# Optimization experiments

Measured on AMD Instinct MI355X. Metric: run time of the kernel, lower is better.

The kernel has to match this reference:

```python
import jax, jax.numpy as jnp
import numpy as np

N = 32768          # nodes
LEVELS = 4         # num_sign_hops + 1
NUM_FEATURES = 512
HIDDEN = 512
VQ_DIM = 64
CODEBOOK_SIZE = 4096
VQ_WEIGHT = 0.25   # commitment_weight


def setup_inputs() -> dict:
    key = jax.random.key(0)
    ks = jax.random.split(key, 11)
    s = 0.02
    return {
        "x": jax.random.normal(ks[0], (N, LEVELS, NUM_FEATURES), jnp.float32),
        # per-level encoder: Linear(F,512) -> ReLU -> Linear(512,D)
        "enc_w1": jax.random.normal(ks[1], (LEVELS, NUM_FEATURES, HIDDEN), jnp.float32) * s,
        "enc_b1": jnp.zeros((LEVELS, HIDDEN), jnp.float32),
        "enc_w2": jax.random.normal(ks[2], (LEVELS, HIDDEN, VQ_DIM), jnp.float32) * s,
        "enc_b2": jnp.zeros((LEVELS, VQ_DIM), jnp.float32),
        # per-level decoder: Linear(D,512) -> ReLU -> Linear(512,F)
        "dec_w1": jax.random.normal(ks[3], (LEVELS, VQ_DIM, HIDDEN), jnp.float32) * s,
        "dec_b1": jnp.zeros((LEVELS, HIDDEN), jnp.float32),
        "dec_w2": jax.random.normal(ks[4], (LEVELS, HIDDEN, NUM_FEATURES), jnp.float32) * s,
        "dec_b2": jnp.zeros((LEVELS, NUM_FEATURES), jnp.float32),
        # per-level EMA codebooks (constants w.r.t. gradient in the torch module)
        "codebook": jax.random.normal(ks[5], (LEVELS, CODEBOOK_SIZE, VQ_DIM), jnp.float32),
    }


def reference(x, enc_w1, enc_b1, enc_w2, enc_b2,
              dec_w1, dec_b1, dec_w2, dec_b2, codebook):
    # Faithful to Quantizer.forward (eval mode: dropout = identity; EMA codebook
    # update is a training-time side effect, not part of the returned math).
    L = x.shape[1]
    total_mse = jnp.float32(0.0)
    commit_last = jnp.float32(0.0)
    for l in range(L):  # small fixed level count, structurally distinct params
        xl = x[:, l, :]                                   # [N, F]
        h = jax.nn.relu(xl @ enc_w1[l] + enc_b1[l])       # [N, 512]
        z = h @ enc_w2[l] + enc_b2[l]                     # [N, D]
        cb = codebook[l]                                  # [K, D]
        # squared euclidean distances [N, K] (cdist^2 via expansion)
        d = ((z * z).sum(-1, keepdims=True)
             - 2.0 * (z @ cb.T)
             + (cb * cb).sum(-1)[None, :])
        idx = jnp.argmin(d, axis=-1)                      # [N]
        q = cb[idx]                                       # [N, D] codebook lookup
        # commitment loss: mse(stop_grad(quantize), z) * weight
        commit = VQ_WEIGHT * jnp.mean((jax.lax.stop_gradient(q) - z) ** 2)
        # straight-through estimator
        quant = z + jax.lax.stop_gradient(q - z)
        h2 = jax.nn.relu(quant @ dec_w1[l] + dec_b1[l])   # [N, 512]
        x_hat = h2 @ dec_w2[l] + dec_b2[l]                # [N, F]
        total_mse = total_mse + jnp.mean((x_hat - xl) ** 2)
        commit_last = commit  # original returns LAST level's commit_loss / levels
    return (total_mse / L, commit_last / L)
```

## Files before the change

### kernel.cpp

```cpp
#include <hip/hip_runtime.h>

#define NS 32768
#define NLEV 4
#define NF 512
#define HID 512
#define VQD 64
#define CBS 4096

typedef __attribute__((ext_vector_type(8))) short bf16x8;
typedef __attribute__((ext_vector_type(4))) float f32x4;

__device__ inline unsigned short f2bf(float f) {
    unsigned int u = __float_as_uint(f);
    unsigned int r = (u + 0x7FFFu + ((u >> 16) & 1u)) >> 16;
    return (unsigned short)r;
}
__device__ inline float bf2f(unsigned short s) {
    return __uint_as_float(((unsigned int)s) << 16);
}

__device__ __forceinline__ void gl16(const void* g, void* l) {
    __builtin_amdgcn_global_load_lds(
        (const __attribute__((address_space(1))) unsigned int*)g,
        (__attribute__((address_space(3))) unsigned int*)l, 16, 0, 0);
}


__global__ void transpose_all(const float* __restrict__ ew1, const float* __restrict__ ew2,
                              const float* __restrict__ dw1, const float* __restrict__ dw2,
                              unsigned short* __restrict__ ew1t, unsigned short* __restrict__ ew2t,
                              unsigned short* __restrict__ dw1t, unsigned short* __restrict__ dw2t) {
    long i = (long)blockIdx.x * 256 + threadIdx.x;
    const long s1 = (long)NLEV * NF * HID;
    const long s2 = (long)NLEV * HID * VQD;
    const long s3 = (long)NLEV * VQD * HID;
    const long s4 = (long)NLEV * HID * NF;
    const float* src;
    unsigned short* dst;
    int R, C;
    if (i < s1) { src = ew1; dst = ew1t; R = NF; C = HID; }
    else if (i < s1 + s2) { i -= s1; src = ew2; dst = ew2t; R = HID; C = VQD; }
    else if (i < s1 + s2 + s3) { i -= s1 + s2; src = dw1; dst = dw1t; R = VQD; C = HID; }
    else if (i < s1 + s2 + s3 + s4) { i -= s1 + s2 + s3; src = dw2; dst = dw2t; R = HID; C = NF; }
    else return;
    int r = (int)(i % R);
    long t = i / R;
    int c = (int)(t % C);
    int b = (int)(t / C);
    dst[i] = f2bf(src[((long)b * R + r) * C + c]);
}

__global__ void cb_prep(const float* __restrict__ cb, unsigned short* __restrict__ cbb,
                        float* __restrict__ cbn) {
    int i = blockIdx.x * 256 + threadIdx.x;
    if (i >= NLEV * CBS) return;
    const float* row = cb + (long)i * VQD;
    float s = 0.f;
    for (int k = 0; k < VQD; k++) {
        float v = row[k];
        s += v * v;
        cbb[(long)i * VQD + k] = f2bf(v);
    }
    cbn[i] = s;
}

__global__ void xconv(const float* __restrict__ x, unsigned short* __restrict__ xb) {
    long i = (long)blockIdx.x * 256 + threadIdx.x;
    int l = (int)(i / ((long)NS * (NF / 8)));
    long rem = i % ((long)NS * (NF / 8));
    int n = (int)(rem >> 6);
    int f8 = ((int)rem & 63) * 8;
    const float* src = x + ((long)n * NLEV + l) * NF + f8;
    float4 f0 = *(const float4*)src;
    float4 f1 = *(const float4*)(src + 4);
    short t[8];
    t[0] = (short)f2bf(f0.x); t[1] = (short)f2bf(f0.y); t[2] = (short)f2bf(f0.z); t[3] = (short)f2bf(f0.w);
    t[4] = (short)f2bf(f1.x); t[5] = (short)f2bf(f1.y); t[6] = (short)f2bf(f1.z); t[7] = (short)f2bf(f1.w);
    *(int4*)(xb + ((long)l * NS + n) * NF + f8) = *(const int4*)t;
}

template <int NT, int NTOT, int RELU, int OUT_MODE, int GATHER>
__global__ __launch_bounds__(256) void gemm128(
    const unsigned short* __restrict__ Ab, long astride, long abatch,
    const int* __restrict__ idx,
    const unsigned short* __restrict__ Bt, long bbatch,
    const float* __restrict__ bias, long biasbatch,
    unsigned short* __restrict__ Cb, long cbatch,
    const unsigned short* __restrict__ Xref, long xbatch,
    float* __restrict__ accum, int K) {
    constexpr int BN = NT * 32;
    constexpr int NPAN = NTOT / BN;
    constexpr int BNP = BN + 8;
    __shared__ __align__(16) short smem[2 * 128 * 32 + 2 * BN * 32];
    short* As = smem;
    short* Bs = smem + 2 * 128 * 32;
    __shared__ float red[4];

    const int bid = blockIdx.x;
    const int inner = bid % (256 * NPAN);
    const int lvl = bid / (256 * NPAN);
    constexpr int CHUNK = 8 * NPAN;
    const int mblk = (inner / CHUNK) * 8 + (inner % CHUNK) / NPAN;
    const int n_blk = inner % NPAN;

    Ab += (long)lvl * abatch;
    Bt += (long)lvl * bbatch;
    bias += (long)lvl * biasbatch;
    if (OUT_MODE == 0) Cb += (long)lvl * cbatch;
    if (OUT_MODE == 2) Xref += (long)lvl * xbatch;
    if (GATHER) idx += (long)lvl * NS;

    const int tid = threadIdx.x;
    const int m0 = mblk * 128;
    const int n0 = n_blk * BN;
    const int wave = tid >> 6, lane = tid & 63, quad = lane >> 4, lr = lane & 15;
    const int wm = wave >> 1, wn = wave & 1;
    const int lrow = lane >> 2;
    const int lcol = (lane & 3) * 8;

    long idx0 = 0, idx1 = 0;
    if (GATHER) {
        idx0 = idx[m0 + wave * 16 + lrow];
        idx1 = idx[m0 + 64 + wave * 16 + lrow];
    }

    f32x4 acc[4][NT];
#pragma unroll
    for (int i = 0; i < 4; i++)
#pragma unroll
        for (int j = 0; j < NT; j++) acc[i][j] = (f32x4){0.f, 0.f, 0.f, 0.f};

    for (int k0 = 0; k0 < K; k0 += 64) {
#pragma unroll
        for (int p = 0; p < 2; p++) {
            const int kk = k0 + p * 32;
            if (GATHER) {
                gl16(Ab + idx0 * K + kk + lcol, &As[p * 4096 + (wave * 16) * 32]);
                gl16(Ab + idx1 * K + kk + lcol, &As[p * 4096 + (64 + wave * 16) * 32]);
            } else {
                const unsigned short* ga = Ab + (long)(m0 + wave * 16 + lrow) * astride + kk + lcol;
                gl16(ga, &As[p * 4096 + (wave * 16) * 32]);
                gl16(ga + 64 * astride, &As[p * 4096 + (64 + wave * 16) * 32]);
            }
            const unsigned short* gb = Bt + (long)(n0 + wave * 16 + lrow) * K + kk + lcol;
            gl16(gb, &Bs[p * BN * 32 + (wave * 16) * 32]);
            if (NT == 4) gl16(gb + 64 * (long)K, &Bs[p * BN * 32 + (64 + wave * 16) * 32]);
        }
        __syncthreads();
#pragma unroll
        for (int p = 0; p < 2; p++) {
            bf16x8 af[4], bfr[NT];
#pragma unroll
            for (int mt = 0; mt < 4; mt++)
                af[mt] = *(const bf16x8*)&As[p * 4096 + (wm * 64 + mt * 16 + lr) * 32 + quad * 8];
#pragma unroll
            for (int nt = 0; nt < NT; nt++)
                bfr[nt] = *(const bf16x8*)&Bs[p * BN * 32 + (wn * NT * 16 + nt * 16 + lr) * 32 + quad * 8];
#pragma unroll
            for (int mt = 0; mt < 4; mt++)
#pragma unroll
                for (int nt = 0; nt < NT; nt++)
                    acc[mt][nt] = __builtin_amdgcn_mfma_f32_16x16x32_bf16(af[mt], bfr[nt], acc[mt][nt], 0, 0, 0);
        }
        __syncthreads();
    }

    float bvs[NT];
#pragma unroll
    for (int nt = 0; nt < NT; nt++) bvs[nt] = bias[n0 + wn * NT * 16 + nt * 16 + lr];

    if (OUT_MODE == 2) {
        float lsum = 0.f;
#pragma unroll
        for (int nt = 0; nt < NT; nt++) {
            int col = n0 + wn * NT * 16 + nt * 16 + lr;
#pragma unroll
            for (int mt = 0; mt < 4; mt++) {
#pragma unroll
                for (int r = 0; r < 4; r++) {
                    int row = m0 + wm * 64 + mt * 16 + quad * 4 + r;
                    float v = acc[mt][nt][r] + bvs[nt];
                    float d = v - bf2f(Xref[(long)row * NTOT + col]);
                    lsum += d * d;
                }
            }
        }
#pragma unroll
        for (int off = 32; off; off >>= 1) lsum += __shfl_down(lsum, off, 64);
        if (lane == 0) red[wave] = lsum;
        __syncthreads();
        if (tid == 0) atomicAdd(accum, red[0] + red[1] + red[2] + red[3]);
    } else {
        short* Ct = smem;
#pragma unroll
        for (int p = 0; p < 2; p++) {
            __syncthreads();
            if (wm == p) {
#pragma unroll
                for (int nt = 0; nt < NT; nt++) {
                    int cl = wn * NT * 16 + nt * 16 + lr;
#pragma unroll
                    for (int mt = 0; mt < 4; mt++) {
#pragma unroll
                        for (int r = 0; r < 4; r++) {
                            int rl = mt * 16 + quad * 4 + r;
                            float v = acc[mt][nt][r] + bvs[nt];
                            if (RELU) v = v > 0.f ? v : 0.f;
                            Ct[rl * BNP + cl] = (short)f2bf(v);
                        }
                    }
                }
            }
            __syncthreads();
            constexpr int PER = (64 * BN / 8) / 256;
#pragma unroll
            for (int j = 0; j < PER; j++) {
                int id = j * 256 + tid;
                int row = id / (BN / 8);
                int seg = id % (BN / 8);
                short tmp[8];
                *(int4*)tmp = *(const int4*)&Ct[row * BNP + seg * 8];
                *(int4*)&Cb[(long)(m0 + p * 64 + row) * NTOT + n0 + seg * 8] = *(const int4*)tmp;
            }
        }
    }
}

__global__ __launch_bounds__(256) void enc2_vq(
    const unsigned short* __restrict__ hb, const unsigned short* __restrict__ ew2t,
    const float* __restrict__ eb2, const unsigned short* __restrict__ cbb,
    const float* __restrict__ cbn, int* __restrict__ idxo, float* __restrict__ accum) {
    __shared__ __align__(16) short As[2 * 128 * 32];
    __shared__ __align__(16) short Bs[2 * 64 * 32];
    __shared__ float znp[2][128];
    __shared__ float zn2[128];
    __shared__ float cred;

    const int lvl = blockIdx.y;
    hb += (long)lvl * NS * HID;
    ew2t += (long)lvl * VQD * HID;
    eb2 += (long)lvl * VQD;
    cbb += (long)lvl * CBS * VQD;
    cbn += (long)lvl * CBS;
    idxo += (long)lvl * NS;

    const int tid = threadIdx.x;
    const int m0 = blockIdx.x * 128;
    const int wave = tid >> 6, lane = tid & 63, quad = lane >> 4, lr = lane & 15;
    const int wm = wave >> 1, wn = wave & 1;
    const int lrow = lane >> 2, lcol = (lane & 3) * 8;

    if (tid == 0) cred = 0.f;

    f32x4 acc[4][2];
#pragma unroll
    for (int i = 0; i < 4; i++)
#pragma unroll
        for (int j = 0; j < 2; j++) acc[i][j] = (f32x4){0.f, 0.f, 0.f, 0.f};

    for (int k0 = 0; k0 < HID; k0 += 64) {
#pragma unroll
        for (int p = 0; p < 2; p++) {
            const int kk = k0 + p * 32;
            const unsigned short* ga = hb + (long)(m0 + wave * 16 + lrow) * HID + kk + lcol;
            gl16(ga, &As[p * 4096 + (wave * 16) * 32]);
            gl16(ga + 64 * HID, &As[p * 4096 + (64 + wave * 16) * 32]);
            const unsigned short* gb = ew2t + (long)(wave * 16 + lrow) * HID + kk + lcol;
            gl16(gb, &Bs[p * 2048 + (wave * 16) * 32]);
        }
        __syncthreads();
#pragma unroll
        for (int p = 0; p < 2; p++) {
            bf16x8 af[4], bfr[2];
#pragma unroll
            for (int mt = 0; mt < 4; mt++)
                af[mt] = *(const bf16x8*)&As[p * 4096 + (wm * 64 + mt * 16 + lr) * 32 + quad * 8];
#pragma unroll
            for (int nt = 0; nt < 2; nt++)
                bfr[nt] = *(const bf16x8*)&Bs[p * 2048 + (wn * 32 + nt * 16 + lr) * 32 + quad * 8];
#pragma unroll
            for (int mt = 0; mt < 4; mt++)
#pragma unroll
                for (int nt = 0; nt < 2; nt++)
                    acc[mt][nt] = __builtin_amdgcn_mfma_f32_16x16x32_bf16(af[mt], bfr[nt], acc[mt][nt], 0, 0, 0);
        }
        __syncthreads();
    }

    short* Zs = As;
    float bvs[2] = {eb2[wn * 32 + lr], eb2[wn * 32 + 16 + lr]};
#pragma unroll
    for (int mt = 0; mt < 4; mt++)
#pragma unroll
        for (int r = 0; r < 4; r++) {
            int row = wm * 64 + mt * 16 + quad * 4 + r;
#pragma unroll
            for (int nt = 0; nt < 2; nt++) {
                float v = acc[mt][nt][r] + bvs[nt];
                Zs[wn * 4096 + row * 32 + nt * 16 + lr] = (short)f2bf(v);
            }
        }
    __syncthreads();

    {
        int row = tid >> 1, p = tid & 1;
        const short* zr = &Zs[p * 4096 + row * 32];
        float s = 0.f;
#pragma unroll
        for (int j = 0; j < 32; j++) {
            float f = bf2f((unsigned short)zr[j]);
            s += f * f;
        }
        znp[p][row] = s;
    }
    bf16x8 a[2][2];
#pragma unroll
    for (int h = 0; h < 2; h++)
#pragma unroll
        for (int p = 0; p < 2; p++)
            a[h][p] = *(const bf16x8*)&Zs[p * 4096 + (h * 64 + wave * 16 + lr) * 32 + quad * 8];
    __syncthreads();
    if (tid < 128) zn2[tid] = znp[0][tid] + znp[1][tid];

    short* Cs = Bs;
    float minv[2][4] = {{1e30f, 1e30f, 1e30f, 1e30f}, {1e30f, 1e30f, 1e30f, 1e30f}};
    int mini[2][4] = {{0, 0, 0, 0}, {0, 0, 0, 0}};

    for (int nb = 0; nb < CBS; nb += 64) {
        __syncthreads();
#pragma unroll
        for (int i = 0; i < 2; i++) {
            int s = i * 4 + wave;
            int p = s >> 2;
            int r0 = (s & 3) * 16;
            gl16(cbb + (long)(nb + r0 + lrow) * VQD + p * 32 + lcol, &Cs[s * 512]);
        }
        __syncthreads();
#pragma unroll
        for (int nt = 0; nt < 4; nt++) {
            bf16x8 b0 = *(const bf16x8*)&Cs[(nt * 16 + lr) * 32 + quad * 8];
            bf16x8 b1 = *(const bf16x8*)&Cs[2048 + (nt * 16 + lr) * 32 + quad * 8];
            int n = nb + nt * 16 + lr;
            float cn = cbn[n];
#pragma unroll
            for (int h = 0; h < 2; h++) {
                f32x4 d4 = {0.f, 0.f, 0.f, 0.f};
                d4 = __builtin_amdgcn_mfma_f32_16x16x32_bf16(a[h][0], b0, d4, 0, 0, 0);
                d4 = __builtin_amdgcn_mfma_f32_16x16x32_bf16(a[h][1], b1, d4, 0, 0, 0);
#pragma unroll
                for (int r = 0; r < 4; r++) {
                    float d = cn - 2.0f * d4[r];
                    if (d < minv[h][r]) {
                        minv[h][r] = d;
                        mini[h][r] = n;
                    }
                }
            }
        }
    }

    float csum = 0.f;
#pragma unroll
    for (int h = 0; h < 2; h++)
#pragma unroll
        for (int r = 0; r < 4; r++) {
            float v = minv[h][r];
            int ix = mini[h][r];
#pragma unroll
            for (int off = 8; off; off >>= 1) {
                float ov = __shfl_xor(v, off, 64);
                int oi = __shfl_xor(ix, off, 64);
                if (ov < v || (ov == v && oi < ix)) {
                    v = ov;
                    ix = oi;
                }
            }
            if (lr == 0) {
                int row = h * 64 + wave * 16 + quad * 4 + r;
                idxo[m0 + row] = ix;
                csum += v + zn2[row];
            }
        }
    if (lvl == NLEV - 1) {
        if (lr == 0) atomicAdd(&cred, csum);
        __syncthreads();
        if (tid == 0) atomicAdd(accum + 1, cred);
    }
}

__global__ void finalize_k(const float* __restrict__ accum, float* __restrict__ out) {
    out[0] = accum[0] / ((float)NS * NF * NLEV);
    out[1] = 0.25f * accum[1] / ((float)NS * VQD * NLEV);
}

extern "C" void kernel_launch(void* const* d_in, const int* in_sizes, int n_in, void* d_out,
                              int out_size, void* d_ws, size_t ws_size, hipStream_t stream) {
    const float* x = (const float*)d_in[0];
    const float* enc_w1 = (const float*)d_in[1];
    const float* enc_b1 = (const float*)d_in[2];
    const float* enc_w2 = (const float*)d_in[3];
    const float* enc_b2 = (const float*)d_in[4];
    const float* dec_w1 = (const float*)d_in[5];
    const float* dec_b1 = (const float*)d_in[6];
    const float* dec_w2 = (const float*)d_in[7];
    const float* dec_b2 = (const float*)d_in[8];
    const float* cb = (const float*)d_in[9];

    char* ws = (char*)d_ws;
    size_t o = 0;
    float* accum = (float*)(ws + o); o += 256;
    unsigned short* enc_w1t = (unsigned short*)(ws + o); o += (size_t)NLEV * HID * NF * 2;
    unsigned short* enc_w2t = (unsigned short*)(ws + o); o += (size_t)NLEV * VQD * HID * 2;
    unsigned short* dec_w1t = (unsigned short*)(ws + o); o += (size_t)NLEV * HID * VQD * 2;
    unsigned short* dec_w2t = (unsigned short*)(ws + o); o += (size_t)NLEV * NF * HID * 2;
    unsigned short* cbb = (unsigned short*)(ws + o); o += (size_t)NLEV * CBS * VQD * 2;
    float* cbn = (float*)(ws + o); o += (size_t)NLEV * CBS * 4;
    unsigned short* xb = (unsigned short*)(ws + o); o += (size_t)NLEV * NS * NF * 2;
    unsigned short* hb = (unsigned short*)(ws + o); o += (size_t)NLEV * NS * HID * 2;
    int* idxp = (int*)(ws + o); o += (size_t)NLEV * NS * 4;

    hipMemsetAsync(accum, 0, 8, stream);

    transpose_all<<<(2 * NLEV * NF * HID + 2 * NLEV * HID * VQD + 255) / 256, 256, 0, stream>>>(
        enc_w1, enc_w2, dec_w1, dec_w2, enc_w1t, enc_w2t, dec_w1t, dec_w2t);
    cb_prep<<<(NLEV * CBS + 255) / 256, 256, 0, stream>>>(cb, cbb, cbn);
    xconv<<<(int)(((long)NLEV * NS * (NF / 8) + 255) / 256), 256, 0, stream>>>(x, xb);

    const int gBig = 256 * (HID / 128) * NLEV;

    gemm128<4, HID, 1, 0, 0><<<gBig, 256, 0, stream>>>(
        xb, NF, (long)NS * NF, nullptr,
        enc_w1t, (long)HID * NF, enc_b1, HID,
        hb, (long)NS * HID, nullptr, 0, nullptr, NF);
    enc2_vq<<<dim3(NS / 128, NLEV), 256, 0, stream>>>(hb, enc_w2t, enc_b2, cbb, cbn, idxp, accum);
    gemm128<4, HID, 1, 0, 1><<<gBig, 256, 0, stream>>>(
        cbb, 0, (long)CBS * VQD, idxp,
        dec_w1t, (long)HID * VQD, dec_b1, HID,
        hb, (long)NS * HID, nullptr, 0, nullptr, VQD);
    gemm128<4, NF, 0, 2, 0><<<gBig, 256, 0, stream>>>(
        hb, HID, (long)NS * HID, nullptr,
        dec_w2t, (long)NF * HID, dec_b2, NF,
        nullptr, 0, xb, (long)NS * NF, accum, HID);

    finalize_k<<<1, 1, 0, stream>>>(accum, (float*)d_out);
}
```

Measured before the change: 835.6 us.

## Fuse encoder MLP+VQ and decoder MLP+loss into two LDS-resident kernels

Replaces the four-kernel GEMM chain with two fused kernels. Each 128-row tile keeps its hidden activations (128x512 bf16) in LDS, so the [N,512] hidden buffer is never written to or read back from global memory. The kernels use 512 threads per block and double-buffered global-to-LDS staging, prefetching the next stage while the current one computes. The cost is 128KB+ of LDS per block, which limits occupancy to one block per CU, and far fewer blocks (1024 per launch) with less latency hiding.

```diff
diff --git a/kernel.cpp b/kernel.cpp
--- a/kernel.cpp
+++ b/kernel.cpp
@@ -9,6 +9,8 @@
 
 typedef __attribute__((ext_vector_type(8))) short bf16x8;
 typedef __attribute__((ext_vector_type(4))) float f32x4;
+
+#define MFMA16(a, b, c) __builtin_amdgcn_mfma_f32_16x16x32_bf16(a, b, c, 0, 0, 0)
 
 __device__ inline unsigned short f2bf(float f) {
     unsigned int u = __float_as_uint(f);
@@ -79,312 +81,323 @@
     *(int4*)(xb + ((long)l * NS + n) * NF + f8) = *(const int4*)t;
 }
 
-template <int NT, int NTOT, int RELU, int OUT_MODE, int GATHER>
-__global__ __launch_bounds__(256) void gemm128(
-    const unsigned short* __restrict__ Ab, long astride, long abatch,
-    const int* __restrict__ idx,
-    const unsigned short* __restrict__ Bt, long bbatch,
-    const float* __restrict__ bias, long biasbatch,
-    unsigned short* __restrict__ Cb, long cbatch,
-    const unsigned short* __restrict__ Xref, long xbatch,
-    float* __restrict__ accum, int K) {
-    constexpr int BN = NT * 32;
-    constexpr int NPAN = NTOT / BN;
-    constexpr int BNP = BN + 8;
-    __shared__ __align__(16) short smem[2 * 128 * 32 + 2 * BN * 32];
-    short* As = smem;
-    short* Bs = smem + 2 * 128 * 32;
-    __shared__ float red[4];
-
-    const int bid = blockIdx.x;
-    const int inner = bid % (256 * NPAN);
-    const int lvl = bid / (256 * NPAN);
-    constexpr int CHUNK = 8 * NPAN;
-    const int mblk = (inner / CHUNK) * 8 + (inner % CHUNK) / NPAN;
-    const int n_blk = inner % NPAN;
-
-    Ab += (long)lvl * abatch;
-    Bt += (long)lvl * bbatch;
-    bias += (long)lvl * biasbatch;
-    if (OUT_MODE == 0) Cb += (long)lvl * cbatch;
-    if (OUT_MODE == 2) Xref += (long)lvl * xbatch;
-    if (GATHER) idx += (long)lvl * NS;
-
-    const int tid = threadIdx.x;
-    const int m0 = mblk * 128;
-    const int n0 = n_blk * BN;
-    const int wave = tid >> 6, lane = tid & 63, quad = lane >> 4, lr = lane & 15;
-    const int wm = wave >> 1, wn = wave & 1;
-    const int lrow = lane >> 2;
-    const int lcol = (lane & 3) * 8;
-
-    long idx0 = 0, idx1 = 0;
-    if (GATHER) {
-        idx0 = idx[m0 + wave * 16 + lrow];
-        idx1 = idx[m0 + 64 + wave * 16 + lrow];
-    }
-
-    f32x4 acc[4][NT];
-#pragma unroll
-    for (int i = 0; i < 4; i++)
-#pragma unroll
-        for (int j = 0; j < NT; j++) acc[i][j] = (f32x4){0.f, 0.f, 0.f, 0.f};
-
-    for (int k0 = 0; k0 < K; k0 += 64) {
-#pragma unroll
-        for (int p = 0; p < 2; p++) {
-            const int kk = k0 + p * 32;
-            if (GATHER) {
-                gl16(Ab + idx0 * K + kk + lcol, &As[p * 4096 + (wave * 16) * 32]);
-                gl16(Ab + idx1 * K + kk + lcol, &As[p * 4096 + (64 + wave * 16) * 32]);
-            } else {
-                const unsigned short* ga = Ab + (long)(m0 + wave * 16 + lrow) * astride + kk + lcol;
-                gl16(ga, &As[p * 4096 + (wave * 16) * 32]);
-                gl16(ga + 64 * astride, &As[p * 4096 + (64 + wave * 16) * 32]);
-            }
-            const unsigned short* gb = Bt + (long)(n0 + wave * 16 + lrow) * K + kk + lcol;
-            gl16(gb, &Bs[p * BN * 32 + (wave * 16) * 32]);
-            if (NT == 4) gl16(gb + 64 * (long)K, &Bs[p * BN * 32 + (64 + wave * 16) * 32]);
-        }
-        __syncthreads();
-#pragma unroll
-        for (int p = 0; p < 2; p++) {
-            bf16x8 af[4], bfr[NT];
-#pragma unroll
-            for (int mt = 0; mt < 4; mt++)
-                af[mt] = *(const bf16x8*)&As[p * 4096 + (wm * 64 + mt * 16 + lr) * 32 + quad * 8];
-#pragma unroll
-            for (int nt = 0; nt < NT; nt++)
-                bfr[nt] = *(const bf16x8*)&Bs[p * BN * 32 + (wn * NT * 16 + nt * 16 + lr) * 32 + quad * 8];
-#pragma unroll
-            for (int mt = 0; mt < 4; mt++)
-#pragma unroll
-                for (int nt = 0; nt < NT; nt++)
-                    acc[mt][nt] = __builtin_amdgcn_mfma_f32_16x16x32_bf16(af[mt], bfr[nt], acc[mt][nt], 0, 0, 0);
-        }
-        __syncthreads();
-    }
-
-    float bvs[NT];
-#pragma unroll
-    for (int nt = 0; nt < NT; nt++) bvs[nt] = bias[n0 + wn * NT * 16 + nt * 16 + lr];
-
-    if (OUT_MODE == 2) {
-        float lsum = 0.f;
-#pragma unroll
-        for (int nt = 0; nt < NT; nt++) {
-            int col = n0 + wn * NT * 16 + nt * 16 + lr;
-#pragma unroll
-            for (int mt = 0; mt < 4; mt++) {
-#pragma unroll
-                for (int r = 0; r < 4; r++) {
-                    int row = m0 + wm * 64 + mt * 16 + quad * 4 + r;
-                    float v = acc[mt][nt][r] + bvs[nt];
-                    float d = v - bf2f(Xref[(long)row * NTOT + col]);
-                    lsum += d * d;
-                }
-            }
-        }
-#pragma unroll
-        for (int off = 32; off; off >>= 1) lsum += __shfl_down(lsum, off, 64);
-        if (lane == 0) red[wave] = lsum;
-        __syncthreads();
-        if (tid == 0) atomicAdd(accum, red[0] + red[1] + red[2] + red[3]);
-    } else {
-        short* Ct = smem;
-#pragma unroll
-        for (int p = 0; p < 2; p++) {
-            __syncthreads();
-            if (wm == p) {
-#pragma unroll
-                for (int nt = 0; nt < NT; nt++) {
-                    int cl = wn * NT * 16 + nt * 16 + lr;
-#pragma unroll
-                    for (int mt = 0; mt < 4; mt++) {
-#pragma unroll
-                        for (int r = 0; r < 4; r++) {
-                            int rl = mt * 16 + quad * 4 + r;
-                            float v = acc[mt][nt][r] + bvs[nt];
-                            if (RELU) v = v > 0.f ? v : 0.f;
-                            Ct[rl * BNP + cl] = (short)f2bf(v);
-                        }
-                    }
-                }
-            }
-            __syncthreads();
-            constexpr int PER = (64 * BN / 8) / 256;
-#pragma unroll
-            for (int j = 0; j < PER; j++) {
-                int id = j * 256 + tid;
-                int row = id / (BN / 8);
-                int seg = id % (BN / 8);
-                short tmp[8];
-                *(int4*)tmp = *(const int4*)&Ct[row * BNP + seg * 8];
-                *(int4*)&Cb[(long)(m0 + p * 64 + row) * NTOT + n0 + seg * 8] = *(const int4*)tmp;
-            }
-        }
-    }
-}
-
-__global__ __launch_bounds__(256) void enc2_vq(
-    const unsigned short* __restrict__ hb, const unsigned short* __restrict__ ew2t,
-    const float* __restrict__ eb2, const unsigned short* __restrict__ cbb,
+__global__ __launch_bounds__(512) void enc_fused(
+    const unsigned short* __restrict__ xb, const unsigned short* __restrict__ w1t,
+    const float* __restrict__ b1, const unsigned short* __restrict__ w2t,
+    const float* __restrict__ b2, const unsigned short* __restrict__ cbb,
     const float* __restrict__ cbn, int* __restrict__ idxo, float* __restrict__ accum) {
-    __shared__ __align__(16) short As[2 * 128 * 32];
-    __shared__ __align__(16) short Bs[2 * 64 * 32];
+    __shared__ __align__(16) short Hs[16 * 4096];
+    __shared__ __align__(16) short Zst[2 * 2048];
     __shared__ float znp[2][128];
     __shared__ float zn2[128];
     __shared__ float cred;
 
     const int lvl = blockIdx.y;
-    hb += (long)lvl * NS * HID;
-    ew2t += (long)lvl * VQD * HID;
-    eb2 += (long)lvl * VQD;
+    const int m0 = blockIdx.x * 128;
+    xb += (long)lvl * NS * NF;
+    w1t += (long)lvl * HID * NF;
+    b1 += (long)lvl * HID;
+    w2t += (long)lvl * VQD * HID;
+    b2 += (long)lvl * VQD;
     cbb += (long)lvl * CBS * VQD;
     cbn += (long)lvl * CBS;
     idxo += (long)lvl * NS;
 
     const int tid = threadIdx.x;
-    const int m0 = blockIdx.x * 128;
     const int wave = tid >> 6, lane = tid & 63, quad = lane >> 4, lr = lane & 15;
-    const int wm = wave >> 1, wn = wave & 1;
-    const int lrow = lane >> 2, lcol = (lane & 3) * 8;
+    const int wm = wave >> 2, wn = wave & 3;
+    const int lrow = lane >> 2;
+    const int lcol = (lane & 3) * 8;
 
     if (tid == 0) cred = 0.f;
 
-    f32x4 acc[4][2];
-#pragma unroll
-    for (int i = 0; i < 4; i++)
-#pragma unroll
-        for (int j = 0; j < 2; j++) acc[i][j] = (f32x4){0.f, 0.f, 0.f, 0.f};
-
-    for (int k0 = 0; k0 < HID; k0 += 64) {
-#pragma unroll
-        for (int p = 0; p < 2; p++) {
-            const int kk = k0 + p * 32;
-            const unsigned short* ga = hb + (long)(m0 + wave * 16 + lrow) * HID + kk + lcol;
-            gl16(ga, &As[p * 4096 + (wave * 16) * 32]);
-            gl16(ga + 64 * HID, &As[p * 4096 + (64 + wave * 16) * 32]);
-            const unsigned short* gb = ew2t + (long)(wave * 16 + lrow) * HID + kk + lcol;
-            gl16(gb, &Bs[p * 2048 + (wave * 16) * 32]);
-        }
-        __syncthreads();
-#pragma unroll
-        for (int p = 0; p < 2; p++) {
-            bf16x8 af[4], bfr[2];
-#pragma unroll
-            for (int mt = 0; mt < 4; mt++)
-                af[mt] = *(const bf16x8*)&As[p * 4096 + (wm * 64 + mt * 16 + lr) * 32 + quad * 8];
-#pragma unroll
-            for (int nt = 0; nt < 2; nt++)
-                bfr[nt] = *(const bf16x8*)&Bs[p * 2048 + (wn * 32 + nt * 16 + lr) * 32 + quad * 8];
-#pragma unroll
-            for (int mt = 0; mt < 4; mt++)
-#pragma unroll
-                for (int nt = 0; nt < 2; nt++)
-                    acc[mt][nt] = __builtin_amdgcn_mfma_f32_16x16x32_bf16(af[mt], bfr[nt], acc[mt][nt], 0, 0, 0);
-        }
-        __syncthreads();
-    }
-
-    short* Zs = As;
-    float bvs[2] = {eb2[wn * 32 + lr], eb2[wn * 32 + 16 + lr]};
-#pragma unroll
-    for (int mt = 0; mt < 4; mt++)
-#pragma unroll
-        for (int r = 0; r < 4; r++) {
-            int row = wm * 64 + mt * 16 + quad * 4 + r;
-#pragma unroll
-            for (int nt = 0; nt < 2; nt++) {
-                float v = acc[mt][nt][r] + bvs[nt];
-                Zs[wn * 4096 + row * 32 + nt * 16 + lr] = (short)f2bf(v);
-            }
-        }
+    f32x4 acc[4][4][2];
+#pragma unroll
+    for (int j = 0; j < 4; j++)
+#pragma unroll
+        for (int mt = 0; mt < 4; mt++) {
+            acc[j][mt][0] = (f32x4){0.f, 0.f, 0.f, 0.f};
+            acc[j][mt][1] = (f32x4){0.f, 0.f, 0.f, 0.f};
+        }
+
+    const unsigned short* ga = xb + (long)(m0 + wave * 16 + lrow) * NF + lcol;
+    auto stage1 = [&](int s) {
+        const int pi = s & 1;
+        gl16(ga + s * 32, &Hs[pi * 4096 + wave * 16 * 32]);
+#pragma unroll
+        for (int j = 0; j < 4; j++)
+            gl16(w1t + (long)(j * 128 + wave * 16 + lrow) * NF + s * 32 + lcol,
+                 &Hs[(2 + 2 * j + pi) * 4096 + wave * 16 * 32]);
+    };
+    stage1(0);
+#pragma unroll 2
+    for (int s = 0; s < 16; s++) {
+        __syncthreads();
+        if (s < 15) stage1(s + 1);
+        const int pi = s & 1;
+        bf16x8 af[4];
+#pragma unroll
+        for (int mt = 0; mt < 4; mt++)
+            af[mt] = *(const bf16x8*)&Hs[pi * 4096 + (wm * 64 + mt * 16 + lr) * 32 + quad * 8];
+#pragma unroll
+        for (int j = 0; j < 4; j++) {
+            bf16x8 bf0 = *(const bf16x8*)&Hs[(2 + 2 * j + pi) * 4096 + (wn * 32 + lr) * 32 + quad * 8];
+            bf16x8 bf1 = *(const bf16x8*)&Hs[(2 + 2 * j + pi) * 4096 + (wn * 32 + 16 + lr) * 32 + quad * 8];
+#pragma unroll
+            for (int mt = 0; mt < 4; mt++) {
+                acc[j][mt][0] = MFMA16(af[mt], bf0, acc[j][mt][0]);
+                acc[j][mt][1] = MFMA16(af[mt], bf1, acc[j][mt][1]);
+            }
+        }
+    }
     __syncthreads();
-
+#pragma unroll
+    for (int j = 0; j < 4; j++) {
+        float bv0 = b1[j * 128 + wn * 32 + lr];
+        float bv1 = b1[j * 128 + wn * 32 + 16 + lr];
+        short* hs = &Hs[(4 * j + wn) * 4096];
+#pragma unroll
+        for (int mt = 0; mt < 4; mt++)
+#pragma unroll
+            for (int r = 0; r < 4; r++) {
+                int row = wm * 64 + mt * 16 + quad * 4 + r;
+                float v0 = acc[j][mt][0][r] + bv0; v0 = v0 > 0.f ? v0 : 0.f;
+                float v1 = acc[j][mt][1][r] + bv1; v1 = v1 > 0.f ? v1 : 0.f;
+                hs[row * 32 + lr] = (short)f2bf(v0);
+                hs[row * 32 + 16 + lr] = (short)f2bf(v1);
+            }
+    }
+
+    f32x4 az[4];
+#pragma unroll
+    for (int mt = 0; mt < 4; mt++) az[mt] = (f32x4){0.f, 0.f, 0.f, 0.f};
+    auto stageZ = [&](int s) {
+        if (wave < 4)
+            gl16(w2t + (long)(wave * 16 + lrow) * HID + s * 32 + lcol,
+                 &Zst[(s & 1) * 2048 + wave * 16 * 32]);
+    };
+    stageZ(0);
+#pragma unroll 2
+    for (int s = 0; s < 16; s++) {
+        __syncthreads();
+        if (s < 15) stageZ(s + 1);
+        bf16x8 bz = *(const bf16x8*)&Zst[(s & 1) * 2048 + (wn * 16 + lr) * 32 + quad * 8];
+#pragma unroll
+        for (int mt = 0; mt < 4; mt++) {
+            bf16x8 af = *(const bf16x8*)&Hs[s * 4096 + (wm * 64 + mt * 16 + lr) * 32 + quad * 8];
+            az[mt] = MFMA16(af, bz, az[mt]);
+        }
+    }
+    __syncthreads();
     {
+        float bz0 = b2[wn * 16 + lr];
+        const int col = wn * 16 + lr;
+        short* zs = &Hs[(col >> 5) * 4096];
+        const int c32 = col & 31;
+#pragma unroll
+        for (int mt = 0; mt < 4; mt++)
+#pragma unroll
+            for (int r = 0; r < 4; r++) {
+                int row = wm * 64 + mt * 16 + quad * 4 + r;
+                zs[row * 32 + c32] = (short)f2bf(az[mt][r] + bz0);
+            }
+    }
+    __syncthreads();
+
+    auto stageC = [&](int t) {
+        gl16(cbb + (long)(t * 64 + wn * 16 + lrow) * VQD + wm * 32 + lcol,
+             &Hs[(2 + (t & 1)) * 4096 + wm * 2048 + wn * 512]);
+    };
+    stageC(0);
+    if (tid < 256) {
         int row = tid >> 1, p = tid & 1;
-        const short* zr = &Zs[p * 4096 + row * 32];
-        float s = 0.f;
-#pragma unroll
-        for (int j = 0; j < 32; j++) {
-            float f = bf2f((unsigned short)zr[j]);
-            s += f * f;
-        }
-        znp[p][row] = s;
-    }
-    bf16x8 a[2][2];
-#pragma unroll
-    for (int h = 0; h < 2; h++)
-#pragma unroll
-        for (int p = 0; p < 2; p++)
-            a[h][p] = *(const bf16x8*)&Zs[p * 4096 + (h * 64 + wave * 16 + lr) * 32 + quad * 8];
+        const short* zr = &Hs[p * 4096 + row * 32];
+        float s2 = 0.f;
+#pragma unroll
+        for (int j2 = 0; j2 < 32; j2++) {
+            float f = bf2f((unsigned short)zr[j2]);
+            s2 += f * f;
+        }
+        znp[p][row] = s2;
+    }
+    bf16x8 a0 = *(const bf16x8*)&Hs[(wave * 16 + lr) * 32 + quad * 8];
+    bf16x8 a1 = *(const bf16x8*)&Hs[4096 + (wave * 16 + lr) * 32 + quad * 8];
     __syncthreads();
     if (tid < 128) zn2[tid] = znp[0][tid] + znp[1][tid];
 
-    short* Cs = Bs;
-    float minv[2][4] = {{1e30f, 1e30f, 1e30f, 1e30f}, {1e30f, 1e30f, 1e30f, 1e30f}};
-    int mini[2][4] = {{0, 0, 0, 0}, {0, 0, 0, 0}};
-
-    for (int nb = 0; nb < CBS; nb += 64) {
-        __syncthreads();
-#pragma unroll
-        for (int i = 0; i < 2; i++) {
-            int s = i * 4 + wave;
-            int p = s >> 2;
-            int r0 = (s & 3) * 16;
-            gl16(cbb + (long)(nb + r0 + lrow) * VQD + p * 32 + lcol, &Cs[s * 512]);
-        }
-        __syncthreads();
+    float minv[4] = {1e30f, 1e30f, 1e30f, 1e30f};
+    int mini[4] = {0, 0, 0, 0};
+#pragma unroll 2
+    for (int t = 0; t < CBS / 64; t++) {
+        if (t) __syncthreads();
+        if (t < CBS / 64 - 1) stageC(t + 1);
+        const short* Cb = &Hs[(2 + (t & 1)) * 4096];
 #pragma unroll
         for (int nt = 0; nt < 4; nt++) {
-            bf16x8 b0 = *(const bf16x8*)&Cs[(nt * 16 + lr) * 32 + quad * 8];
-            bf16x8 b1 = *(const bf16x8*)&Cs[2048 + (nt * 16 + lr) * 32 + quad * 8];
-            int n = nb + nt * 16 + lr;
+            bf16x8 c0 = *(const bf16x8*)&Cb[(nt * 16 + lr) * 32 + quad * 8];
+            bf16x8 c1 = *(const bf16x8*)&Cb[2048 + (nt * 16 + lr) * 32 + quad * 8];
+            f32x4 d4 = {0.f, 0.f, 0.f, 0.f};
+            d4 = MFMA16(a0, c0, d4);
+            d4 = MFMA16(a1, c1, d4);
+            int n = t * 64 + nt * 16 + lr;
             float cn = cbn[n];
 #pragma unroll
-            for (int h = 0; h < 2; h++) {
-                f32x4 d4 = {0.f, 0.f, 0.f, 0.f};
-                d4 = __builtin_amdgcn_mfma_f32_16x16x32_bf16(a[h][0], b0, d4, 0, 0, 0);
-                d4 = __builtin_amdgcn_mfma_f32_16x16x32_bf16(a[h][1], b1, d4, 0, 0, 0);
-#pragma unroll
-                for (int r = 0; r < 4; r++) {
-                    float d = cn - 2.0f * d4[r];
-                    if (d < minv[h][r]) {
-                        minv[h][r] = d;
-                        mini[h][r] = n;
-                    }
-                }
+            for (int r = 0; r < 4; r++) {
+                float d = fmaf(-2.f, d4[r], cn);
+                if (d < minv[r]) { minv[r] = d; mini[r] = n; }
             }
         }
     }
 
     float csum = 0.f;
 #pragma unroll
-    for (int h = 0; h < 2; h++)
-#pragma unroll
-        for (int r = 0; r < 4; r++) {
-            float v = minv[h][r];
-            int ix = mini[h][r];
-#pragma unroll
-            for (int off = 8; off; off >>= 1) {
-                float ov = __shfl_xor(v, off, 64);
-                int oi = __shfl_xor(ix, off, 64);
-                if (ov < v || (ov == v && oi < ix)) {
-                    v = ov;
-                    ix = oi;
-                }
-            }
-            if (lr == 0) {
-                int row = h * 64 + wave * 16 + quad * 4 + r;
-                idxo[m0 + row] = ix;
-                csum += v + zn2[row];
-            }
-        }
+    for (int r = 0; r < 4; r++) {
+        float v = minv[r];
+        int ix = mini[r];
+#pragma unroll
+        for (int off = 8; off; off >>= 1) {
+            float ov = __shfl_xor(v, off, 64);
+            int oi = __shfl_xor(ix, off, 64);
+            if (ov < v || (ov == v && oi < ix)) { v = ov; ix = oi; }
+        }
+        if (lr == 0) {
+            int row = wave * 16 + quad * 4 + r;
+            idxo[m0 + row] = ix;
+            csum += v + zn2[row];
+        }
+    }
     if (lvl == NLEV - 1) {
         if (lr == 0) atomicAdd(&cred, csum);
         __syncthreads();
         if (tid == 0) atomicAdd(accum + 1, cred);
+    }
+}
+
+__global__ __launch_bounds__(512) void dec_fused(
+    const unsigned short* __restrict__ cbb, const int* __restrict__ idx,
+    const unsigned short* __restrict__ w1t, const float* __restrict__ b1,
+    const unsigned short* __restrict__ w2t, const float* __restrict__ b2,
+    const unsigned short* __restrict__ xref, float* __restrict__ accum) {
+    __shared__ __align__(16) short Hs[16 * 4096];
+    __shared__ __align__(16) short Bst[2 * 4096];
+    __shared__ float red[8];
+
+    const int lvl = blockIdx.y;
+    const int m0 = blockIdx.x * 128;
+    cbb += (long)lvl * CBS * VQD;
+    idx += (long)lvl * NS;
+    w1t += (long)lvl * HID * VQD;
+    b1 += (long)lvl * HID;
+    w2t += (long)lvl * NF * HID;
+    b2 += (long)lvl * NF;
+    xref += (long)lvl * NS * NF;
+
+    const int tid = threadIdx.x;
+    const int wave = tid >> 6, lane = tid & 63, quad = lane >> 4, lr = lane & 15;
+    const int wm = wave >> 2, wn = wave & 3;
+    const int lrow = lane >> 2;
+    const int lcol = (lane & 3) * 8;
+
+    const long idxv = idx[m0 + wave * 16 + lrow];
+
+    auto stageD = [&](int j) {
+#pragma unroll
+        for (int p = 0; p < 2; p++) {
+            gl16(cbb + idxv * VQD + p * 32 + lcol, &Hs[(4 * j + p) * 4096 + wave * 16 * 32]);
+            gl16(w1t + (long)(j * 128 + wave * 16 + lrow) * VQD + p * 32 + lcol,
+                 &Hs[(4 * j + 2 + p) * 4096 + wave * 16 * 32]);
+        }
+    };
+    stageD(0);
+#pragma unroll
+    for (int j = 0; j < 4; j++) {
+        f32x4 acc[4][2];
+#pragma unroll
+        for (int mt = 0; mt < 4; mt++) {
+            acc[mt][0] = (f32x4){0.f, 0.f, 0.f, 0.f};
+            acc[mt][1] = (f32x4){0.f, 0.f, 0.f, 0.f};
+        }
+        __syncthreads();
+        if (j < 3) stageD(j + 1);
+#pragma unroll
+        for (int p = 0; p < 2; p++) {
+            bf16x8 bf0 = *(const bf16x8*)&Hs[(4 * j + 2 + p) * 4096 + (wn * 32 + lr) * 32 + quad * 8];
+            bf16x8 bf1 = *(const bf16x8*)&Hs[(4 * j + 2 + p) * 4096 + (wn * 32 + 16 + lr) * 32 + quad * 8];
+#pragma unroll
+            for (int mt = 0; mt < 4; mt++) {
+                bf16x8 af = *(const bf16x8*)&Hs[(4 * j + p) * 4096 + (wm * 64 + mt * 16 + lr) * 32 + quad * 8];
+                acc[mt][0] = MFMA16(af, bf0, acc[mt][0]);
+                acc[mt][1] = MFMA16(af, bf1, acc[mt][1]);
+            }
+        }
+        __syncthreads();
+        float bv0 = b1[j * 128 + wn * 32 + lr];
+        float bv1 = b1[j * 128 + wn * 32 + 16 + lr];
+        short* hs = &Hs[(4 * j + wn) * 4096];
+#pragma unroll
+        for (int mt = 0; mt < 4; mt++)
+#pragma unroll
+            for (int r = 0; r < 4; r++) {
+                int row = wm * 64 + mt * 16 + quad * 4 + r;
+                float v0 = acc[mt][0][r] + bv0; v0 = v0 > 0.f ? v0 : 0.f;
+                float v1 = acc[mt][1][r] + bv1; v1 = v1 > 0.f ? v1 : 0.f;
+                hs[row * 32 + lr] = (short)f2bf(v0);
+                hs[row * 32 + 16 + lr] = (short)f2bf(v1);
+            }
+    }
+
+    auto stageB = [&](int g) {
+        gl16(w2t + (long)((g >> 4) * 128 + wave * 16 + lrow) * HID + (g & 15) * 32 + lcol,
+             &Bst[(g & 1) * 4096 + wave * 16 * 32]);
+    };
+    stageB(0);
+    float lsum = 0.f;
+    f32x4 acc2[4][2];
+#pragma unroll
+    for (int mt = 0; mt < 4; mt++) {
+        acc2[mt][0] = (f32x4){0.f, 0.f, 0.f, 0.f};
+        acc2[mt][1] = (f32x4){0.f, 0.f, 0.f, 0.f};
+    }
+#pragma unroll 2
+    for (int g = 0; g < 64; g++) {
+        __syncthreads();
+        if (g < 63) stageB(g + 1);
+        const int s = g & 15;
+        bf16x8 bf0 = *(const bf16x8*)&Bst[(g & 1) * 4096 + (wn * 32 + lr) * 32 + quad * 8];
+        bf16x8 bf1 = *(const bf16x8*)&Bst[(g & 1) * 4096 + (wn * 32 + 16 + lr) * 32 + quad * 8];
+#pragma unroll
+        for (int mt = 0; mt < 4; mt++) {
+            bf16x8 af = *(const bf16x8*)&Hs[s * 4096 + (wm * 64 + mt * 16 + lr) * 32 + quad * 8];
+            acc2[mt][0] = MFMA16(af, bf0, acc2[mt][0]);
+            acc2[mt][1] = MFMA16(af, bf1, acc2[mt][1]);
+        }
+        if (s == 15) {
+            const int jj = g >> 4;
+            float bv0 = b2[jj * 128 + wn * 32 + lr];
+            float bv1 = b2[jj * 128 + wn * 32 + 16 + lr];
+#pragma unroll
+            for (int mt = 0; mt < 4; mt++)
+#pragma unroll
+                for (int r = 0; r < 4; r++) {
+                    long row = m0 + wm * 64 + mt * 16 + quad * 4 + r;
+                    int c0 = jj * 128 + wn * 32 + lr;
+                    float v0 = acc2[mt][0][r] + bv0 - bf2f(xref[row * NF + c0]);
+                    float v1 = acc2[mt][1][r] + bv1 - bf2f(xref[row * NF + c0 + 16]);
+                    lsum += v0 * v0 + v1 * v1;
+                    acc2[mt][0][r] = 0.f;
+                    acc2[mt][1][r] = 0.f;
+                }
+        }
+    }
+#pragma unroll
+    for (int off = 32; off; off >>= 1) lsum += __shfl_down(lsum, off, 64);
+    if (lane == 0) red[wave] = lsum;
+    __syncthreads();
+    if (tid == 0) {
+        float s2 = 0.f;
+#pragma unroll
+        for (int w = 0; w < 8; w++) s2 += red[w];
+        atomicAdd(accum, s2);
     }
 }
 
@@ -416,7 +429,6 @@
     unsigned short* cbb = (unsigned short*)(ws + o); o += (size_t)NLEV * CBS * VQD * 2;
     float* cbn = (float*)(ws + o); o += (size_t)NLEV * CBS * 4;
     unsigned short* xb = (unsigned short*)(ws + o); o += (size_t)NLEV * NS * NF * 2;
-    unsigned short* hb = (unsigned short*)(ws + o); o += (size_t)NLEV * NS * HID * 2;
     int* idxp = (int*)(ws + o); o += (size_t)NLEV * NS * 4;
 
     hipMemsetAsync(accum, 0, 8, stream);
@@ -426,21 +438,10 @@
     cb_prep<<<(NLEV * CBS + 255) / 256, 256, 0, stream>>>(cb, cbb, cbn);
     xconv<<<(int)(((long)NLEV * NS * (NF / 8) + 255) / 256), 256, 0, stream>>>(x, xb);
 
-    const int gBig = 256 * (HID / 128) * NLEV;
-
-    gemm128<4, HID, 1, 0, 0><<<gBig, 256, 0, stream>>>(
-        xb, NF, (long)NS * NF, nullptr,
-        enc_w1t, (long)HID * NF, enc_b1, HID,
-        hb, (long)NS * HID, nullptr, 0, nullptr, NF);
-    enc2_vq<<<dim3(NS / 128, NLEV), 256, 0, stream>>>(hb, enc_w2t, enc_b2, cbb, cbn, idxp, accum);
-    gemm128<4, HID, 1, 0, 1><<<gBig, 256, 0, stream>>>(
-        cbb, 0, (long)CBS * VQD, idxp,
-        dec_w1t, (long)HID * VQD, dec_b1, HID,
-        hb, (long)NS * HID, nullptr, 0, nullptr, VQD);
-    gemm128<4, NF, 0, 2, 0><<<gBig, 256, 0, stream>>>(
-        hb, HID, (long)NS * HID, nullptr,
-        dec_w2t, (long)NF * HID, dec_b2, NF,
-        nullptr, 0, xb, (long)NS * NF, accum, HID);
+    enc_fused<<<dim3(NS / 128, NLEV), 512, 0, stream>>>(
+        xb, enc_w1t, enc_b1, enc_w2t, enc_b2, cbb, cbn, idxp, accum);
+    dec_fused<<<dim3(NS / 128, NLEV), 512, 0, stream>>>(
+        cbb, idxp, dec_w1t, dec_b1, dec_w2t, dec_b2, xb, accum);
 
     finalize_k<<<1, 1, 0, stream>>>(accum, (float*)d_out);
 }
```

New measurement: 989.1 us. 1.18x slower.

## Fuse encoder layer-1 GEMM into enc2/VQ kernel, keeping hidden tiles in LDS

Applied to the files above, without the earlier changes.

Replaces the separate encoder first-layer GEMM and enc2_vq kernels with one fused kernel. Each block computes 128-column hidden chunks of ReLU(x W1 + b1) into LDS and immediately accumulates them into z, so the bf16 hidden activation never goes to global memory. The LDS tiles use an XOR-swizzled layout to avoid bank conflicts, and the codebook loop is double-buffered. The distance search is reformulated as an argmax of z·c − ‖c‖²/2, with the bias folded into the MFMA accumulator init. In exchange the fused kernel has one block per 128 rows, so it launches fewer blocks than the old layer-1 GEMM, and larger LDS use may limit occupancy.

```diff
diff --git a/kernel.cpp b/kernel.cpp
--- a/kernel.cpp
+++ b/kernel.cpp
@@ -9,6 +9,8 @@
 
 typedef __attribute__((ext_vector_type(8))) short bf16x8;
 typedef __attribute__((ext_vector_type(4))) float f32x4;
+
+#define MFMA16(a, b, c) __builtin_amdgcn_mfma_f32_16x16x32_bf16(a, b, c, 0, 0, 0)
 
 __device__ inline unsigned short f2bf(float f) {
     unsigned int u = __float_as_uint(f);
@@ -226,134 +228,214 @@
     }
 }
 
-__global__ __launch_bounds__(256) void enc2_vq(
-    const unsigned short* __restrict__ hb, const unsigned short* __restrict__ ew2t,
-    const float* __restrict__ eb2, const unsigned short* __restrict__ cbb,
+__global__ __launch_bounds__(256, 3) void enc_fused(
+    const unsigned short* __restrict__ xb, const unsigned short* __restrict__ w1t,
+    const float* __restrict__ b1, const unsigned short* __restrict__ w2t,
+    const float* __restrict__ b2, const unsigned short* __restrict__ cbb,
     const float* __restrict__ cbn, int* __restrict__ idxo, float* __restrict__ accum) {
-    __shared__ __align__(16) short As[2 * 128 * 32];
-    __shared__ __align__(16) short Bs[2 * 64 * 32];
+    __shared__ __align__(16) char SM[49152];
     __shared__ float znp[2][128];
     __shared__ float zn2[128];
     __shared__ float cred;
 
+    char* AsB = SM;
+    char* BsB = SM + 16384;
+    char* HpB = SM;
+    char* ZsB = SM + 32768;
+    char* CsB = SM;
+
     const int lvl = blockIdx.y;
-    hb += (long)lvl * NS * HID;
-    ew2t += (long)lvl * VQD * HID;
-    eb2 += (long)lvl * VQD;
+    const int m0 = blockIdx.x * 128;
+    xb += (long)lvl * NS * NF;
+    w1t += (long)lvl * HID * NF;
+    b1 += (long)lvl * HID;
+    w2t += (long)lvl * VQD * HID;
+    b2 += (long)lvl * VQD;
     cbb += (long)lvl * CBS * VQD;
     cbn += (long)lvl * CBS;
     idxo += (long)lvl * NS;
 
     const int tid = threadIdx.x;
-    const int m0 = blockIdx.x * 128;
     const int wave = tid >> 6, lane = tid & 63, quad = lane >> 4, lr = lane & 15;
     const int wm = wave >> 1, wn = wave & 1;
-    const int lrow = lane >> 2, lcol = (lane & 3) * 8;
 
     if (tid == 0) cred = 0.f;
 
-    f32x4 acc[4][2];
-#pragma unroll
-    for (int i = 0; i < 4; i++)
-#pragma unroll
-        for (int j = 0; j < 2; j++) acc[i][j] = (f32x4){0.f, 0.f, 0.f, 0.f};
-
-    for (int k0 = 0; k0 < HID; k0 += 64) {
-#pragma unroll
-        for (int p = 0; p < 2; p++) {
-            const int kk = k0 + p * 32;
-            const unsigned short* ga = hb + (long)(m0 + wave * 16 + lrow) * HID + kk + lcol;
-            gl16(ga, &As[p * 4096 + (wave * 16) * 32]);
-            gl16(ga + 64 * HID, &As[p * 4096 + (64 + wave * 16) * 32]);
-            const unsigned short* gb = ew2t + (long)(wave * 16 + lrow) * HID + kk + lcol;
-            gl16(gb, &Bs[p * 2048 + (wave * 16) * 32]);
-        }
-        __syncthreads();
-#pragma unroll
-        for (int p = 0; p < 2; p++) {
-            bf16x8 af[4], bfr[2];
+    f32x4 az[4][2];
+#pragma unroll
+    for (int mt = 0; mt < 4; mt++) {
+        az[mt][0] = (f32x4){0.f, 0.f, 0.f, 0.f};
+        az[mt][1] = (f32x4){0.f, 0.f, 0.f, 0.f};
+    }
+
+    for (int j = 0; j < 4; j++) {
+#pragma unroll
+        for (int c = 0; c < 4; c++) {
+            int q = c * 256 + tid;
+            int row = q >> 4;
+            int ch = (q & 15) ^ (row & 7);
+            gl16(w2t + (long)row * HID + j * 128 + ch * 8, ZsB + c * 4096 + wave * 1024);
+        }
+        f32x4 acc[4][4];
+#pragma unroll
+        for (int mt = 0; mt < 4; mt++)
+#pragma unroll
+            for (int nt = 0; nt < 4; nt++) acc[mt][nt] = (f32x4){0.f, 0.f, 0.f, 0.f};
+
+        for (int step = 0; step < 8; step++) {
+            const int k0 = step * 64;
+#pragma unroll
+            for (int c = 0; c < 4; c++) {
+                int q = c * 256 + tid;
+                int row = q >> 3;
+                int kk = ((q & 7) ^ (row & 7)) * 8;
+                gl16(xb + (long)(m0 + row) * NF + k0 + kk, AsB + c * 4096 + wave * 1024);
+            }
+#pragma unroll
+            for (int c = 0; c < 4; c++) {
+                int q = c * 256 + tid;
+                int row = q >> 3;
+                int kk = ((q & 7) ^ (row & 7)) * 8;
+                gl16(w1t + (long)(j * 128 + row) * NF + k0 + kk, BsB + c * 4096 + wave * 1024);
+            }
+            __syncthreads();
+#pragma unroll
+            for (int p = 0; p < 2; p++) {
+                bf16x8 af[4], bf[4];
+#pragma unroll
+                for (int mt = 0; mt < 4; mt++) {
+                    int row = wm * 64 + mt * 16 + lr;
+                    af[mt] = *(const bf16x8*)(AsB + row * 128 + ((p * 64 + quad * 16) ^ ((row & 7) << 4)));
+                }
+#pragma unroll
+                for (int nt = 0; nt < 4; nt++) {
+                    int row = wn * 64 + nt * 16 + lr;
+                    bf[nt] = *(const bf16x8*)(BsB + row * 128 + ((p * 64 + quad * 16) ^ ((row & 7) << 4)));
+                }
+#pragma unroll
+                for (int mt = 0; mt < 4; mt++)
+#pragma unroll
+                    for (int nt = 0; nt < 4; nt++)
+                        acc[mt][nt] = MFMA16(af[mt], bf[nt], acc[mt][nt]);
+            }
+            __syncthreads();
+        }
+#pragma unroll
+        for (int nt = 0; nt < 4; nt++) {
+            int col = wn * 64 + nt * 16 + lr;
+            float bv = b1[j * 128 + col];
 #pragma unroll
             for (int mt = 0; mt < 4; mt++)
-                af[mt] = *(const bf16x8*)&As[p * 4096 + (wm * 64 + mt * 16 + lr) * 32 + quad * 8];
-#pragma unroll
-            for (int nt = 0; nt < 2; nt++)
-                bfr[nt] = *(const bf16x8*)&Bs[p * 2048 + (wn * 32 + nt * 16 + lr) * 32 + quad * 8];
+#pragma unroll
+                for (int r = 0; r < 4; r++) {
+                    int row = wm * 64 + mt * 16 + quad * 4 + r;
+                    float v = acc[mt][nt][r] + bv;
+                    v = v > 0.f ? v : 0.f;
+                    *(short*)(HpB + row * 256 + ((col * 2) ^ ((row & 7) << 4))) = (short)f2bf(v);
+                }
+        }
+        __syncthreads();
+#pragma unroll
+        for (int s = 0; s < 4; s++) {
+            bf16x8 ah[4], w2f[2];
+#pragma unroll
+            for (int mt = 0; mt < 4; mt++) {
+                int row = wm * 64 + mt * 16 + lr;
+                ah[mt] = *(const bf16x8*)(HpB + row * 256 + ((s * 64 + quad * 16) ^ ((row & 7) << 4)));
+            }
+#pragma unroll
+            for (int nt = 0; nt < 2; nt++) {
+                int row = wn * 32 + nt * 16 + lr;
+                w2f[nt] = *(const bf16x8*)(ZsB + row * 256 + ((s * 64 + quad * 16) ^ ((row & 7) << 4)));
+            }
 #pragma unroll
             for (int mt = 0; mt < 4; mt++)
 #pragma unroll
                 for (int nt = 0; nt < 2; nt++)
-                    acc[mt][nt] = __builtin_amdgcn_mfma_f32_16x16x32_bf16(af[mt], bfr[nt], acc[mt][nt], 0, 0, 0);
-        }
-        __syncthreads();
-    }
-
-    short* Zs = As;
-    float bvs[2] = {eb2[wn * 32 + lr], eb2[wn * 32 + 16 + lr]};
-#pragma unroll
-    for (int mt = 0; mt < 4; mt++)
-#pragma unroll
-        for (int r = 0; r < 4; r++) {
-            int row = wm * 64 + mt * 16 + quad * 4 + r;
-#pragma unroll
-            for (int nt = 0; nt < 2; nt++) {
-                float v = acc[mt][nt][r] + bvs[nt];
-                Zs[wn * 4096 + row * 32 + nt * 16 + lr] = (short)f2bf(v);
-            }
-        }
+                    az[mt][nt] = MFMA16(ah[mt], w2f[nt], az[mt][nt]);
+        }
+        __syncthreads();
+    }
+
+#pragma unroll
+    for (int nt = 0; nt < 2; nt++) {
+        int col = wn * 32 + nt * 16 + lr;
+        float bz = b2[col];
+#pragma unroll
+        for (int mt = 0; mt < 4; mt++)
+#pragma unroll
+            for (int r = 0; r < 4; r++) {
+                int row = wm * 64 + mt * 16 + quad * 4 + r;
+                float v = az[mt][nt][r] + bz;
+                *(short*)(ZsB + row * 128 + ((col * 2) ^ ((row & 7) << 4))) = (short)f2bf(v);
+            }
+    }
     __syncthreads();
 
+#pragma unroll
+    for (int c = 0; c < 2; c++) {
+        int q = c * 256 + tid;
+        int row = q >> 3;
+        int kk = ((q & 7) ^ (row & 7)) * 8;
+        gl16(cbb + (long)row * VQD + kk, CsB + c * 4096 + wave * 1024);
+    }
     {
         int row = tid >> 1, p = tid & 1;
-        const short* zr = &Zs[p * 4096 + row * 32];
-        float s = 0.f;
-#pragma unroll
-        for (int j = 0; j < 32; j++) {
-            float f = bf2f((unsigned short)zr[j]);
-            s += f * f;
-        }
-        znp[p][row] = s;
+        float s2 = 0.f;
+#pragma unroll
+        for (int c = 0; c < 4; c++) {
+            bf16x8 v = *(const bf16x8*)(ZsB + row * 128 + ((p * 64 + c * 16) ^ ((row & 7) << 4)));
+#pragma unroll
+            for (int e = 0; e < 8; e++) {
+                float f = bf2f((unsigned short)v[e]);
+                s2 += f * f;
+            }
+        }
+        znp[p][row] = s2;
     }
     bf16x8 a[2][2];
 #pragma unroll
     for (int h = 0; h < 2; h++)
 #pragma unroll
-        for (int p = 0; p < 2; p++)
-            a[h][p] = *(const bf16x8*)&Zs[p * 4096 + (h * 64 + wave * 16 + lr) * 32 + quad * 8];
+        for (int p = 0; p < 2; p++) {
+            int row = h * 64 + wave * 16 + lr;
+            a[h][p] = *(const bf16x8*)(ZsB + row * 128 + ((p * 64 + quad * 16) ^ ((row & 7) << 4)));
+        }
     __syncthreads();
     if (tid < 128) zn2[tid] = znp[0][tid] + znp[1][tid];
 
-    short* Cs = Bs;
-    float minv[2][4] = {{1e30f, 1e30f, 1e30f, 1e30f}, {1e30f, 1e30f, 1e30f, 1e30f}};
-    int mini[2][4] = {{0, 0, 0, 0}, {0, 0, 0, 0}};
-
-    for (int nb = 0; nb < CBS; nb += 64) {
-        __syncthreads();
-#pragma unroll
-        for (int i = 0; i < 2; i++) {
-            int s = i * 4 + wave;
-            int p = s >> 2;
-            int r0 = (s & 3) * 16;
-            gl16(cbb + (long)(nb + r0 + lrow) * VQD + p * 32 + lcol, &Cs[s * 512]);
-        }
-        __syncthreads();
+    float maxv[2][4] = {{-1e30f, -1e30f, -1e30f, -1e30f}, {-1e30f, -1e30f, -1e30f, -1e30f}};
+    int maxi[2][4] = {{0, 0, 0, 0}, {0, 0, 0, 0}};
+#pragma unroll 2
+    for (int t = 0; t < CBS / 64; t++) {
+        __syncthreads();
+        if (t < CBS / 64 - 1) {
+#pragma unroll
+            for (int c = 0; c < 2; c++) {
+                int q = c * 256 + tid;
+                int row = q >> 3;
+                int kk = ((q & 7) ^ (row & 7)) * 8;
+                gl16(cbb + (long)((t + 1) * 64 + row) * VQD + kk,
+                     CsB + ((t + 1) & 1) * 8192 + c * 4096 + wave * 1024);
+            }
+        }
+        const char* Cbuf = CsB + (t & 1) * 8192;
 #pragma unroll
         for (int nt = 0; nt < 4; nt++) {
-            bf16x8 b0 = *(const bf16x8*)&Cs[(nt * 16 + lr) * 32 + quad * 8];
-            bf16x8 b1 = *(const bf16x8*)&Cs[2048 + (nt * 16 + lr) * 32 + quad * 8];
-            int n = nb + nt * 16 + lr;
+            int rowc = nt * 16 + lr;
+            int n = t * 64 + rowc;
             float cn = cbn[n];
+            bf16x8 c0 = *(const bf16x8*)(Cbuf + rowc * 128 + ((quad * 16) ^ ((rowc & 7) << 4)));
+            bf16x8 c1 = *(const bf16x8*)(Cbuf + rowc * 128 + ((64 + quad * 16) ^ ((rowc & 7) << 4)));
+            float ci = -0.5f * cn;
 #pragma unroll
             for (int h = 0; h < 2; h++) {
-                f32x4 d4 = {0.f, 0.f, 0.f, 0.f};
-                d4 = __builtin_amdgcn_mfma_f32_16x16x32_bf16(a[h][0], b0, d4, 0, 0, 0);
-                d4 = __builtin_amdgcn_mfma_f32_16x16x32_bf16(a[h][1], b1, d4, 0, 0, 0);
+                f32x4 d4 = {ci, ci, ci, ci};
+                d4 = MFMA16(a[h][0], c0, d4);
+                d4 = MFMA16(a[h][1], c1, d4);
 #pragma unroll
                 for (int r = 0; r < 4; r++) {
-                    float d = cn - 2.0f * d4[r];
-                    if (d < minv[h][r]) {
-                        minv[h][r] = d;
-                        mini[h][r] = n;
-                    }
+                    if (d4[r] > maxv[h][r]) { maxv[h][r] = d4[r]; maxi[h][r] = n; }
                 }
             }
         }
@@ -364,21 +446,18 @@
     for (int h = 0; h < 2; h++)
 #pragma unroll
         for (int r = 0; r < 4; r++) {
-            float v = minv[h][r];
-            int ix = mini[h][r];
+            float v = maxv[h][r];
+            int ix = maxi[h][r];
 #pragma unroll
             for (int off = 8; off; off >>= 1) {
                 float ov = __shfl_xor(v, off, 64);
                 int oi = __shfl_xor(ix, off, 64);
-                if (ov < v || (ov == v && oi < ix)) {
-                    v = ov;
-                    ix = oi;
-                }
+                if (ov > v || (ov == v && oi < ix)) { v = ov; ix = oi; }
             }
             if (lr == 0) {
                 int row = h * 64 + wave * 16 + quad * 4 + r;
                 idxo[m0 + row] = ix;
-                csum += v + zn2[row];
+                csum += fmaf(-2.f, v, zn2[row]);
             }
         }
     if (lvl == NLEV - 1) {
@@ -426,13 +505,10 @@
     cb_prep<<<(NLEV * CBS + 255) / 256, 256, 0, stream>>>(cb, cbb, cbn);
     xconv<<<(int)(((long)NLEV * NS * (NF / 8) + 255) / 256), 256, 0, stream>>>(x, xb);
 
+    enc_fused<<<dim3(NS / 128, NLEV), 256, 0, stream>>>(
+        xb, enc_w1t, enc_b1, enc_w2t, enc_b2, cbb, cbn, idxp, accum);
+
     const int gBig = 256 * (HID / 128) * NLEV;
-
-    gemm128<4, HID, 1, 0, 0><<<gBig, 256, 0, stream>>>(
-        xb, NF, (long)NS * NF, nullptr,
-        enc_w1t, (long)HID * NF, enc_b1, HID,
-        hb, (long)NS * HID, nullptr, 0, nullptr, NF);
-    enc2_vq<<<dim3(NS / 128, NLEV), 256, 0, stream>>>(hb, enc_w2t, enc_b2, cbb, cbn, idxp, accum);
     gemm128<4, HID, 1, 0, 1><<<gBig, 256, 0, stream>>>(
         cbb, 0, (long)CBS * VQD, idxp,
         dec_w1t, (long)HID * VQD, dec_b1, HID,
```

Measured after the change: 1.089 ms. 30.3% more time.
